# Kernel tuning notes

Hardware: AMD Instinct MI355X
Metric: run time of the kernel (lower is better)

## Reference

```python
import jax, jax.numpy as jnp
import numpy as np

N_NODES = 50000
N_EDGES = 1000000
IN_C = 64
OUT_C = 64
N_TYPES = 4


def setup_inputs() -> dict:
    key = jax.random.key(0)
    k_x, k_ei, k_et, k_w, k_rw, k_rb = jax.random.split(key, 6)
    x = jax.random.normal(k_x, (N_NODES, IN_C), dtype=jnp.float32)
    edge_index = jax.random.randint(k_ei, (2, N_EDGES), 0, N_NODES, dtype=jnp.int64)
    edge_type = jax.random.randint(k_et, (N_EDGES,), 0, N_TYPES, dtype=jnp.int64)
    # xavier_uniform for weight: bound = sqrt(6/(in+out))
    bound_w = float(np.sqrt(6.0 / (IN_C + OUT_C)))
    weight = jax.random.uniform(k_w, (N_TYPES, IN_C, OUT_C), minval=-bound_w, maxval=bound_w, dtype=jnp.float32)
    # nn.Linear default init: kaiming_uniform-ish, U(-1/sqrt(in), 1/sqrt(in))
    bound_l = float(1.0 / np.sqrt(IN_C))
    root_w = jax.random.uniform(k_rw, (IN_C, OUT_C), minval=-bound_l, maxval=bound_l, dtype=jnp.float32)
    root_b = jax.random.uniform(k_rb, (OUT_C,), minval=-bound_l, maxval=bound_l, dtype=jnp.float32)
    return {"x": x, "edge_index": edge_index, "edge_type": edge_type,
            "weight": weight, "root_w": root_w, "root_b": root_b}


def reference(x, edge_index, edge_type, weight, root_w, root_b):
    src, dst = edge_index[0], edge_index[1]
    x_src = x[src]                                   # [E, in]
    # Per-type GEMM + masked select; avoids materializing weight[edge_type] ([E,in,out]).
    msgs = jnp.zeros((x_src.shape[0], weight.shape[2]), dtype=x.dtype)
    for t in range(weight.shape[0]):                 # small fixed type count
        sel = (edge_type == t)[:, None]
        msgs = msgs + jnp.where(sel, x_src @ weight[t], 0.0)
    # Scatter-add messages to destination nodes.
    agg = jax.ops.segment_sum(msgs, dst, num_segments=x.shape[0])  # [N, out]
    return agg + x @ root_w + root_b
```

## Files before the change

### kernel.cpp

```cpp
#include <hip/hip_runtime.h>

#define NT 64
#define NBMAX1 1024
#define CAPB 2048
#define CHUNK 4096
#define FTHR 512

typedef short bf16x8 __attribute__((ext_vector_type(8)));
typedef float f32x4  __attribute__((ext_vector_type(4)));

__device__ __forceinline__ unsigned short f2bf(float f) {
    unsigned u = __builtin_bit_cast(unsigned, f);
    unsigned r = (u + 0x7fffu + ((u >> 16) & 1u)) >> 16;
    return (unsigned short)r;
}
__device__ __forceinline__ float bf2f(unsigned short h) {
    return __builtin_bit_cast(float, (unsigned)h << 16);
}
__device__ __forceinline__ unsigned pack2(float a, float b) {
    return (unsigned)f2bf(a) | ((unsigned)f2bf(b) << 16);
}

__global__ __launch_bounds__(FTHR) void ph_kernel(
    const float* __restrict__ weight, const float* __restrict__ root_w,
    unsigned short* __restrict__ wt,
    const int* __restrict__ ei, int* __restrict__ counts,
    int n_edges, int nb, int nblk)
{
    const int tid = threadIdx.x;
    int g = blockIdx.x * FTHR + tid;
    if (g < 5 * 4096) {
        int m = g >> 12, rem = g & 4095, c = rem >> 6, k = rem & 63;
        float v = (m < 4) ? weight[m * 4096 + k * 64 + c] : root_w[k * 64 + c];
        int byte = m * 8192 + c * 128 + ((k * 2) ^ ((c & 7) << 4));
        wt[byte >> 1] = f2bf(v);
    }
    if (blockIdx.x >= nblk) return;

    __shared__ int lh[NBMAX1];
    for (int i = tid; i < nb; i += FTHR) lh[i] = 0;
    __syncthreads();
    const int lo = blockIdx.x * CHUNK;
    const int hi = min(lo + CHUNK, n_edges);
    for (int e = lo + tid; e < hi; e += FTHR)
        atomicAdd(&lh[ei[n_edges + e] >> 6], 1);
    __syncthreads();
    for (int i = tid; i < nb; i += FTHR)
        counts[(size_t)blockIdx.x * nb + i] = lh[i];
}

__global__ __launch_bounds__(256) void scanw_kernel(
    const int* __restrict__ counts, int* __restrict__ starts,
    int* __restrict__ cursor, int nb, int nblk)
{
    if (blockIdx.x == 0 && threadIdx.x == 0) cursor[nb] = 0;
    const int w    = (blockIdx.x * 256 + threadIdx.x) >> 6;
    const int lane = threadIdx.x & 63;
    if (w >= nb) return;
    const int b = w;
    int base = 0;
    for (int r = 0; r * 64 < nblk; ++r) {
        int i = r * 64 + lane;
        int c = (i < nblk) ? counts[(size_t)i * nb + b] : 0;
        int s = c;
        #pragma unroll
        for (int d = 1; d < 64; d <<= 1) {
            int u = __shfl_up(s, d, 64);
            if (lane >= d) s += u;
        }
        if (i < nblk) starts[(size_t)i * nb + b] = base + s - c;
        base += __shfl(s, 63, 64);
    }
    if (lane == 0) cursor[b] = base;
}

__global__ __launch_bounds__(FTHR) void fused_fg_kernel(
    const float* __restrict__ x, const uint4* __restrict__ wt4,
    const float* __restrict__ root_b,
    float* __restrict__ out, unsigned short* __restrict__ y, int n_nodes,
    const int* __restrict__ ei, const int* __restrict__ et,
    const int* __restrict__ starts, int* __restrict__ cursor,
    int2* __restrict__ spill, unsigned* __restrict__ payload,
    int n_edges, int nb, int nblk, int ssh, int tsh)
{
    __shared__ __align__(16) char smem[57344];
    const int tid = threadIdx.x;

    if (blockIdx.x < nblk) {
        unsigned*       pl   = (unsigned*)smem;
        unsigned short* bkt  = (unsigned short*)(pl + CHUNK);
        int*            lh   = (int*)(bkt + CHUNK);
        int*            loff = lh + NBMAX1;
        int*            tsum = loff + NBMAX1 + 1;

        const int blk = blockIdx.x;
        const int lo  = blk * CHUNK;
        const int hi  = min(lo + CHUNK, n_edges);
        const int n   = hi - lo;

        for (int i = tid; i < nb; i += FTHR) lh[i] = 0;
        __syncthreads();
        for (int i = tid; i < n; i += FTHR)
            atomicAdd(&lh[ei[n_edges + lo + i] >> 6], 1);
        __syncthreads();

        const int bins  = (nb + FTHR - 1) / FTHR;
        const int base_ = tid * bins;
        int s = 0;
        for (int j = 0; j < bins; ++j) {
            int idx = base_ + j;
            if (idx < nb) s += lh[idx];
        }
        tsum[tid] = s;
        __syncthreads();
        for (int d = 1; d < FTHR; d <<= 1) {
            int v = (tid >= d) ? tsum[tid - d] : 0;
            __syncthreads();
            tsum[tid] += v;
            __syncthreads();
        }
        int run = (tid == 0) ? 0 : tsum[tid - 1];
        for (int j = 0; j < bins; ++j) {
            int idx = base_ + j;
            if (idx < nb) { loff[idx] = run; run += lh[idx]; }
        }
        __syncthreads();
        for (int i = tid; i < nb; i += FTHR) lh[i] = 0;
        __syncthreads();

        for (int i = tid; i < n; i += FTHR) {
            int e   = lo + i;
            int src = ei[e];
            int dn  = ei[n_edges + e];
            int t   = et[e];
            int b   = dn >> 6;
            int r   = atomicAdd(&lh[b], 1);
            int slot = loff[b] + r;
            pl[slot]  = (unsigned)src | ((unsigned)(dn & 63) << ssh)
                      | ((unsigned)t << tsh);
            bkt[slot] = (unsigned short)b;
        }
        __syncthreads();

        const int* __restrict__ srow = starts + (size_t)blk * nb;
        for (int i = tid; i < n; i += FTHR) {
            int b    = bkt[i];
            int rank = srow[b] + (i - loff[b]);
            unsigned v = pl[i];
            if (rank < CAPB) {
                payload[(size_t)b * CAPB + rank] = v;
            } else {
                int sp = atomicAdd(&cursor[nb], 1);
                spill[sp] = make_int2(b, (int)v);
            }
        }
        return;
    }

    uint4* lds4 = (uint4*)smem;
    const int node0 = (blockIdx.x - nblk) * 128;

    for (int i = tid; i < 2560; i += FTHR) lds4[1024 + i] = wt4[i];

    {
        int n    = tid >> 2;
        int kq   = tid & 3;
        int node = node0 + n;
        uint4 p0, p1;
        if (node < n_nodes) {
            const float4* src = reinterpret_cast<const float4*>(x)
                                + (size_t)node * 16 + kq * 4;
            float4 f0 = src[0], f1 = src[1], f2 = src[2], f3 = src[3];
            p0.x = pack2(f0.x, f0.y); p0.y = pack2(f0.z, f0.w);
            p0.z = pack2(f1.x, f1.y); p0.w = pack2(f1.z, f1.w);
            p1.x = pack2(f2.x, f2.y); p1.y = pack2(f2.z, f2.w);
            p1.z = pack2(f3.x, f3.y); p1.w = pack2(f3.z, f3.w);
        } else {
            p0 = make_uint4(0, 0, 0, 0);
            p1 = p0;
        }
        int s0 = (kq * 2) ^ (n & 7);
        lds4[n * 8 + s0]       = p0;
        lds4[n * 8 + (s0 ^ 1)] = p1;
    }
    __syncthreads();

    const int wv = tid >> 6;
    const int l  = tid & 63;
    const int lo = l & 15;
    const int hi = l >> 4;

    const int arow = (wv >> 2) * 64 + (wv & 3) * 16 + lo;
    bf16x8 xb0 = *reinterpret_cast<const bf16x8*>(
        &lds4[arow * 8 + ((0 + hi) ^ (arow & 7))]);
    bf16x8 xb1 = *reinterpret_cast<const bf16x8*>(
        &lds4[arow * 8 + ((4 + hi) ^ (arow & 7))]);

    const int node   = node0 + arow;
    const bool valid = (node < n_nodes);

    for (int m = 0; m < 5; ++m) {
        f32x4 acc[4];
        #pragma unroll
        for (int j = 0; j < 4; ++j)
            acc[j] = (f32x4){0.f, 0.f, 0.f, 0.f};

        #pragma unroll
        for (int j = 0; j < 4; ++j) {
            int c     = j * 16 + lo;
            int bbase = 1024 + m * 512 + c * 8;
            bf16x8 w0 = *reinterpret_cast<const bf16x8*>(
                &lds4[bbase + ((0 + hi) ^ (c & 7))]);
            acc[j] = __builtin_amdgcn_mfma_f32_16x16x32_bf16(w0, xb0, acc[j], 0, 0, 0);
            bf16x8 w1 = *reinterpret_cast<const bf16x8*>(
                &lds4[bbase + ((4 + hi) ^ (c & 7))]);
            acc[j] = __builtin_amdgcn_mfma_f32_16x16x32_bf16(w1, xb1, acc[j], 0, 0, 0);
        }

        if (m < 4) {
            if (valid) {
                unsigned short* __restrict__ ym = y + (size_t)m * n_nodes * 64;
                #pragma unroll
                for (int j = 0; j < 4; ++j) {
                    uint2 o;
                    o.x = pack2(acc[j][0], acc[j][1]);
                    o.y = pack2(acc[j][2], acc[j][3]);
                    *reinterpret_cast<uint2*>(
                        &ym[(size_t)node * 64 + j * 16 + hi * 4]) = o;
                }
            }
        } else {
            if (valid) {
                #pragma unroll
                for (int j = 0; j < 4; ++j) {
                    float4 rb = reinterpret_cast<const float4*>(root_b)[j * 4 + hi];
                    float4 o  = make_float4(acc[j][0] + rb.x, acc[j][1] + rb.y,
                                            acc[j][2] + rb.z, acc[j][3] + rb.w);
                    *reinterpret_cast<float4*>(
                        &out[(size_t)node * 64 + j * 16 + hi * 4]) = o;
                }
            }
        }
    }
}

__global__ __launch_bounds__(1024) void gatherb5_kernel(
    const int* __restrict__ cursor, const unsigned* __restrict__ payload,
    const int2* __restrict__ spill,
    const unsigned short* __restrict__ y, float* __restrict__ out,
    int n_nodes, int nb, int ssh, int tsh)
{
    __shared__ unsigned raw[CAPB];
    __shared__ unsigned srt[CAPB];
    __shared__ int hist[64];
    __shared__ int hoff[65];

    const int tid = threadIdx.x;
    const int b   = blockIdx.x;
    const int n_in = min(cursor[b], CAPB);
    const unsigned* __restrict__ pl_base = payload + (size_t)b * CAPB;

    if (tid < 64) hist[tid] = 0;
    __syncthreads();
    for (int i = tid; i < n_in; i += 1024) {
        unsigned pl = pl_base[i];
        raw[i] = pl;
        atomicAdd(&hist[(pl >> ssh) & 63], 1);
    }
    __syncthreads();
    if (tid < 64) {
        int v = hist[tid];
        int s = v;
        #pragma unroll
        for (int d = 1; d < 64; d <<= 1) {
            int u = __shfl_up(s, d, 64);
            if (tid >= d) s += u;
        }
        hoff[tid] = s - v;
        if (tid == 63) hoff[64] = s;
        hist[tid] = 0;
    }
    __syncthreads();
    for (int i = tid; i < n_in; i += 1024) {
        unsigned pl = raw[i];
        int lnode = (pl >> ssh) & 63;
        int r = atomicAdd(&hist[lnode], 1);
        srt[hoff[lnode] + r] = pl;
    }
    __syncthreads();

    const int g    = tid >> 4;
    const int cq   = tid & 15;
    const int node = b * 64 + g;
    const unsigned smask = (1u << ssh) - 1;
    const ushort4* __restrict__ y4 = reinterpret_cast<const ushort4*>(y);

    float4 acc = make_float4(0.f, 0.f, 0.f, 0.f);
    const int s0 = hoff[g];
    const int s1 = hoff[g + 1];
    int p = s0;
    for (; p + 1 < s1; p += 2) {
        unsigned pl0 = srt[p];
        unsigned pl1 = srt[p + 1];
        ushort4 v0 = y4[((long)(pl0 >> tsh) * n_nodes + (pl0 & smask)) * 16 + cq];
        ushort4 v1 = y4[((long)(pl1 >> tsh) * n_nodes + (pl1 & smask)) * 16 + cq];
        acc.x += bf2f(v0.x) + bf2f(v1.x);
        acc.y += bf2f(v0.y) + bf2f(v1.y);
        acc.z += bf2f(v0.z) + bf2f(v1.z);
        acc.w += bf2f(v0.w) + bf2f(v1.w);
    }
    if (p < s1) {
        unsigned pl = srt[p];
        ushort4 v = y4[((long)(pl >> tsh) * n_nodes + (pl & smask)) * 16 + cq];
        acc.x += bf2f(v.x); acc.y += bf2f(v.y);
        acc.z += bf2f(v.z); acc.w += bf2f(v.w);
    }

    const int S = cursor[nb];
    for (int i = 0; i < S; ++i) {
        int2 sp = spill[i];
        if (sp.x == b) {
            unsigned v = (unsigned)sp.y;
            if ((int)((v >> ssh) & 63) == g) {
                int src = (int)(v & smask);
                int t   = (int)(v >> tsh);
                ushort4 w = y4[((long)t * n_nodes + src) * 16 + cq];
                acc.x += bf2f(w.x); acc.y += bf2f(w.y);
                acc.z += bf2f(w.z); acc.w += bf2f(w.w);
            }
        }
    }

    if (node < n_nodes) {
        float4* o  = reinterpret_cast<float4*>(out) + (long)node * 16 + cq;
        float4 cur = *o;
        cur.x += acc.x; cur.y += acc.y; cur.z += acc.z; cur.w += acc.w;
        *o = cur;
    }
}

__global__ __launch_bounds__(256) void gemm_fused2_kernel(
    const float* __restrict__ x, const float* __restrict__ weight,
    const float* __restrict__ root_w, const float* __restrict__ root_b,
    float* __restrict__ out, unsigned short* __restrict__ y, int n_nodes)
{
    __shared__ unsigned short xsT[64][72];
    __shared__ float ws[64][72];
    const int tid   = threadIdx.x;
    const int node0 = blockIdx.x * 64;
    #pragma unroll
    for (int i = 0; i < 4; ++i) {
        int v    = tid + i * 256;
        int r    = v >> 4;
        int cq   = v & 15;
        int node = node0 + r;
        float4 x4 = (node < n_nodes)
                        ? reinterpret_cast<const float4*>(x)[(size_t)node * 16 + cq]
                        : make_float4(0.f, 0.f, 0.f, 0.f);
        xsT[cq * 4 + 0][r] = f2bf(x4.x);
        xsT[cq * 4 + 1][r] = f2bf(x4.y);
        xsT[cq * 4 + 2][r] = f2bf(x4.z);
        xsT[cq * 4 + 3][r] = f2bf(x4.w);
    }
    const int ng = tid & 31;
    const int cg = tid >> 5;
    float bias[8];
    #pragma unroll
    for (int j = 0; j < 8; ++j) bias[j] = root_b[cg * 8 + j];
    for (int m = 0; m < 5; ++m) {
        const float* __restrict__ W = (m < 4) ? (weight + m * 4096) : root_w;
        __syncthreads();
        #pragma unroll
        for (int i = 0; i < 4; ++i) {
            int v  = tid + i * 256;
            int r  = v >> 4;
            int cq = v & 15;
            float4 w4 = reinterpret_cast<const float4*>(W)[v];
            ws[r][cq * 4 + 0] = w4.x; ws[r][cq * 4 + 1] = w4.y;
            ws[r][cq * 4 + 2] = w4.z; ws[r][cq * 4 + 3] = w4.w;
        }
        __syncthreads();
        float acc[2][8];
        #pragma unroll
        for (int i = 0; i < 2; ++i)
            #pragma unroll
            for (int j = 0; j < 8; ++j) acc[i][j] = 0.f;
        #pragma unroll 4
        for (int k = 0; k < 64; ++k) {
            unsigned xu = *reinterpret_cast<const unsigned*>(&xsT[k][ng * 2]);
            float xv0 = __builtin_bit_cast(float, xu << 16);
            float xv1 = __builtin_bit_cast(float, xu & 0xffff0000u);
            float4 wa = *reinterpret_cast<const float4*>(&ws[k][cg * 8]);
            float4 wb = *reinterpret_cast<const float4*>(&ws[k][cg * 8 + 4]);
            float wv[8] = {wa.x, wa.y, wa.z, wa.w, wb.x, wb.y, wb.z, wb.w};
            #pragma unroll
            for (int j = 0; j < 8; ++j) {
                acc[0][j] += xv0 * wv[j];
                acc[1][j] += xv1 * wv[j];
            }
        }
        #pragma unroll
        for (int i = 0; i < 2; ++i) {
            int node = node0 + ng * 2 + i;
            if (node >= n_nodes) continue;
            if (m < 4) {
                uint4 o;
                o.x = pack2(acc[i][0], acc[i][1]);
                o.y = pack2(acc[i][2], acc[i][3]);
                o.z = pack2(acc[i][4], acc[i][5]);
                o.w = pack2(acc[i][6], acc[i][7]);
                *reinterpret_cast<uint4*>(
                    &y[((size_t)m * n_nodes + node) * 64 + cg * 8]) = o;
            } else {
                float4 oa = make_float4(acc[i][0] + bias[0], acc[i][1] + bias[1],
                                        acc[i][2] + bias[2], acc[i][3] + bias[3]);
                float4 ob = make_float4(acc[i][4] + bias[4], acc[i][5] + bias[5],
                                        acc[i][6] + bias[6], acc[i][7] + bias[7]);
                reinterpret_cast<float4*>(&out[(size_t)node * 64 + cg * 8])[0] = oa;
                reinterpret_cast<float4*>(&out[(size_t)node * 64 + cg * 8])[1] = ob;
            }
        }
    }
}

__global__ __launch_bounds__(256) void scatter_kernel(
    const int* __restrict__ ei, const int* __restrict__ et,
    const unsigned short* __restrict__ y, float* __restrict__ out,
    int n_edges, int n_nodes)
{
    long idx = (long)blockIdx.x * blockDim.x + threadIdx.x;
    if (idx >= (long)n_edges * 16) return;
    int e  = (int)(idx >> 4);
    int cq = (int)(idx & 15);
    int src  = ei[e];
    int dstn = ei[n_edges + e];
    int t    = et[e];
    ushort4 v = reinterpret_cast<const ushort4*>(y)[((long)t * n_nodes + src) * 16 + cq];
    float* o = out + (long)dstn * 64 + cq * 4;
    atomicAdd(o + 0, bf2f(v.x));
    atomicAdd(o + 1, bf2f(v.y));
    atomicAdd(o + 2, bf2f(v.z));
    atomicAdd(o + 3, bf2f(v.w));
}

__global__ __launch_bounds__(256) void gemm_root_kernel(
    const float* __restrict__ x, const float* __restrict__ root_w,
    const float* __restrict__ root_b, float* __restrict__ out, int n_nodes)
{
    __shared__ float xs[NT][65];
    __shared__ float ws[64][65];
    const int tid   = threadIdx.x;
    const int node0 = blockIdx.x * NT;
    #pragma unroll
    for (int i = 0; i < 4; ++i) {
        int v  = tid + i * 256;
        int r  = v >> 4;
        int cq = v & 15;
        float4 w4 = reinterpret_cast<const float4*>(root_w)[v];
        ws[r][cq * 4 + 0] = w4.x; ws[r][cq * 4 + 1] = w4.y;
        ws[r][cq * 4 + 2] = w4.z; ws[r][cq * 4 + 3] = w4.w;
        int node = node0 + r;
        float4 x4 = (node < n_nodes)
                        ? reinterpret_cast<const float4*>(x)[node * 16 + cq]
                        : make_float4(0.f, 0.f, 0.f, 0.f);
        xs[r][cq * 4 + 0] = x4.x; xs[r][cq * 4 + 1] = x4.y;
        xs[r][cq * 4 + 2] = x4.z; xs[r][cq * 4 + 3] = x4.w;
    }
    __syncthreads();
    const int tc = (tid & 15) * 4;
    const int tr = (tid >> 4) * 4;
    float acc[4][4];
    #pragma unroll
    for (int i = 0; i < 4; ++i)
        #pragma unroll
        for (int j = 0; j < 4; ++j) acc[i][j] = 0.f;
    #pragma unroll 4
    for (int k = 0; k < 64; ++k) {
        float xv[4], wv[4];
        #pragma unroll
        for (int i = 0; i < 4; ++i) xv[i] = xs[tr + i][k];
        #pragma unroll
        for (int j = 0; j < 4; ++j) wv[j] = ws[k][tc + j];
        #pragma unroll
        for (int i = 0; i < 4; ++i)
            #pragma unroll
            for (int j = 0; j < 4; ++j) acc[i][j] += xv[i] * wv[j];
    }
    #pragma unroll
    for (int i = 0; i < 4; ++i) {
        int node = node0 + tr + i;
        if (node < n_nodes) {
            float4 o = make_float4(acc[i][0] + root_b[tc + 0], acc[i][1] + root_b[tc + 1],
                                   acc[i][2] + root_b[tc + 2], acc[i][3] + root_b[tc + 3]);
            reinterpret_cast<float4*>(out)[node * 16 + (tc >> 2)] = o;
        }
    }
}

__global__ __launch_bounds__(256) void edge_direct_kernel(
    const float* __restrict__ x, const int* __restrict__ ei,
    const int* __restrict__ et, const float* __restrict__ weight,
    float* __restrict__ out, int n_edges)
{
    int gwave  = (int)((blockIdx.x * (long)blockDim.x + threadIdx.x) >> 6);
    int lane   = threadIdx.x & 63;
    int nwaves = (int)(((long)gridDim.x * blockDim.x) >> 6);
    for (int e = gwave; e < n_edges; e += nwaves) {
        int src  = ei[e];
        int dstn = ei[n_edges + e];
        int t    = et[e];
        float xv = x[src * 64 + lane];
        const float* __restrict__ W = weight + t * 4096;
        float acc = 0.f;
        #pragma unroll 8
        for (int k = 0; k < 64; ++k) {
            float xk = __shfl(xv, k);
            acc += xk * W[k * 64 + lane];
        }
        atomicAdd(&out[(long)dstn * 64 + lane], acc);
    }
}

extern "C" void kernel_launch(void* const* d_in, const int* in_sizes, int n_in,
                              void* d_out, int out_size, void* d_ws, size_t ws_size,
                              hipStream_t stream) {
    const float* x      = (const float*)d_in[0];
    const int*   ei     = (const int*)d_in[1];
    const int*   et     = (const int*)d_in[2];
    const float* weight = (const float*)d_in[3];
    const float* root_w = (const float*)d_in[4];
    const float* root_b = (const float*)d_in[5];
    float* out = (float*)d_out;

    const int n_nodes = in_sizes[0] / 64;
    const int n_edges = in_sizes[2];
    const int nb      = (n_nodes + 63) >> 6;
    const int nblk    = (n_edges + CHUNK - 1) / CHUNK;

    int ssh = 1;
    while ((1 << ssh) < n_nodes) ++ssh;
    const int tsh = ssh + 6;

    const size_t wt_bytes = 5 * 4096 * sizeof(unsigned short);
    const size_t y_bytes  = (size_t)4 * n_nodes * 64 * sizeof(unsigned short);
    const size_t b_bytes  = wt_bytes + y_bytes +
        ((size_t)nb + 1 + 2 * (size_t)nblk * nb + (size_t)nb * CAPB
         + 2 * (size_t)n_edges) * 4;

    const int gemm_blocks = (n_nodes + 127) / 128;

    if (nb <= NBMAX1 && tsh + 2 <= 32 && ws_size >= b_bytes) {
        unsigned short* wt      = (unsigned short*)d_ws;
        unsigned short* y       = (unsigned short*)((char*)d_ws + wt_bytes);
        int*            cursor  = (int*)((char*)d_ws + wt_bytes + y_bytes);
        int*            counts  = cursor + nb + 1;
        int*            starts  = counts + (size_t)nblk * nb;
        unsigned*       payload = (unsigned*)(starts + (size_t)nblk * nb);
        int2*           spill   = (int2*)(payload + (size_t)nb * CAPB);

        const int ph_blocks = max(nblk, (5 * 4096 + FTHR - 1) / FTHR);
        ph_kernel<<<ph_blocks, FTHR, 0, stream>>>(
            weight, root_w, wt, ei, counts, n_edges, nb, nblk);
        scanw_kernel<<<(nb * 64 + 255) / 256, 256, 0, stream>>>(
            counts, starts, cursor, nb, nblk);
        fused_fg_kernel<<<nblk + gemm_blocks, FTHR, 0, stream>>>(
            x, (const uint4*)wt, root_b, out, y, n_nodes,
            ei, et, starts, cursor, spill, payload,
            n_edges, nb, nblk, ssh, tsh);
        gatherb5_kernel<<<nb, 1024, 0, stream>>>(
            cursor, payload, spill, y, out, n_nodes, nb, ssh, tsh);
    } else if (ws_size >= y_bytes) {
        unsigned short* y = (unsigned short*)d_ws;
        gemm_fused2_kernel<<<(n_nodes + 63) / 64, 256, 0, stream>>>(
            x, weight, root_w, root_b, out, y, n_nodes);
        long total  = (long)n_edges * 16;
        int  blocks = (int)((total + 255) / 256);
        scatter_kernel<<<blocks, 256, 0, stream>>>(ei, et, y, out, n_edges, n_nodes);
    } else {
        gemm_root_kernel<<<(n_nodes + NT - 1) / NT, 256, 0, stream>>>(
            x, root_w, root_b, out, n_nodes);
        edge_direct_kernel<<<4096, 256, 0, stream>>>(x, ei, et, weight, out, n_edges);
    }
}
```

Before: 65.14 us.

## Fuse four-kernel pipeline into one cooperative persistent kernel with grid syncs

Replaces the four launches (histogram/weight prep, scan, bucket+GEMM, gather) with a single cooperative mega-kernel that loops over work items and uses grid.sync between phases. The aim is to remove launch gaps and tail effects between the dependent stages. In exchange the grid is capped at 512 persistent blocks, so each block handles several chunks serially. The gather phase now uses 512 threads per bucket instead of 1024, and the grid barriers add their own cost. The launch path also makes several host-side attribute and occupancy queries on every call.

```diff
diff --git a/kernel.cpp b/kernel.cpp
--- a/kernel.cpp
+++ b/kernel.cpp
@@ -1,4 +1,6 @@
 #include <hip/hip_runtime.h>
+#include <hip/hip_cooperative_groups.h>
+namespace cg = cooperative_groups;
 
 #define NT 64
 #define NBMAX1 1024
@@ -19,6 +21,327 @@
 }
 __device__ __forceinline__ unsigned pack2(float a, float b) {
     return (unsigned)f2bf(a) | ((unsigned)f2bf(b) << 16);
+}
+
+__global__ __launch_bounds__(FTHR) void mega_kernel(
+    const float* x, const float* weight, const float* root_w,
+    const float* root_b, float* out, unsigned short* wt,
+    unsigned short* y, const int* ei, const int* et,
+    int* counts, int* starts, int* cursor, int2* spill,
+    unsigned* payload, int n_nodes, int n_edges, int nb, int nblk,
+    int gemm_tiles, int ssh, int tsh)
+{
+    cg::grid_group grid = cg::this_grid();
+    __shared__ __align__(16) char smem[57344];
+    const int tid  = threadIdx.x;
+    const int nthr = gridDim.x * FTHR;
+
+    for (int g = blockIdx.x * FTHR + tid; g < 5 * 4096; g += nthr) {
+        int m = g >> 12, rem = g & 4095, c = rem >> 6, k = rem & 63;
+        float v = (m < 4) ? weight[m * 4096 + k * 64 + c] : root_w[k * 64 + c];
+        int byte = m * 8192 + c * 128 + ((k * 2) ^ ((c & 7) << 4));
+        wt[byte >> 1] = f2bf(v);
+    }
+    if (blockIdx.x == 0 && tid == 0) cursor[nb] = 0;
+    {
+        int* lh = (int*)smem;
+        for (int c = blockIdx.x; c < nblk; c += gridDim.x) {
+            __syncthreads();
+            for (int i = tid; i < nb; i += FTHR) lh[i] = 0;
+            __syncthreads();
+            const int lo = c * CHUNK;
+            const int hi = min(lo + CHUNK, n_edges);
+            for (int e = lo + tid; e < hi; e += FTHR)
+                atomicAdd(&lh[ei[n_edges + e] >> 6], 1);
+            __syncthreads();
+            for (int i = tid; i < nb; i += FTHR)
+                counts[(size_t)c * nb + i] = lh[i];
+        }
+    }
+    grid.sync();
+
+    {
+        const int lane = tid & 63;
+        for (int b = blockIdx.x * 8 + (tid >> 6); b < nb; b += gridDim.x * 8) {
+            int base = 0;
+            for (int r = 0; r * 64 < nblk; ++r) {
+                int i = r * 64 + lane;
+                int c = (i < nblk) ? counts[(size_t)i * nb + b] : 0;
+                int s = c;
+                #pragma unroll
+                for (int d = 1; d < 64; d <<= 1) {
+                    int u = __shfl_up(s, d, 64);
+                    if (lane >= d) s += u;
+                }
+                if (i < nblk) starts[(size_t)i * nb + b] = base + s - c;
+                base += __shfl(s, 63, 64);
+            }
+            if (lane == 0) cursor[b] = base;
+        }
+    }
+    grid.sync();
+
+    const int nit = nblk + gemm_tiles;
+    for (int it = blockIdx.x; it < nit; it += gridDim.x) {
+        __syncthreads();
+        if (it < nblk) {
+            unsigned*       pl   = (unsigned*)smem;
+            unsigned short* bkt  = (unsigned short*)(pl + CHUNK);
+            int*            lh   = (int*)(bkt + CHUNK);
+            int*            loff = lh + NBMAX1;
+            int*            tsum = loff + NBMAX1 + 1;
+
+            const int blk = it;
+            const int lo  = blk * CHUNK;
+            const int hi  = min(lo + CHUNK, n_edges);
+            const int n   = hi - lo;
+
+            for (int i = tid; i < nb; i += FTHR) lh[i] = 0;
+            __syncthreads();
+            for (int i = tid; i < n; i += FTHR)
+                atomicAdd(&lh[ei[n_edges + lo + i] >> 6], 1);
+            __syncthreads();
+
+            const int bins  = (nb + FTHR - 1) / FTHR;
+            const int base_ = tid * bins;
+            int s = 0;
+            for (int j = 0; j < bins; ++j) {
+                int idx = base_ + j;
+                if (idx < nb) s += lh[idx];
+            }
+            tsum[tid] = s;
+            __syncthreads();
+            for (int d = 1; d < FTHR; d <<= 1) {
+                int v = (tid >= d) ? tsum[tid - d] : 0;
+                __syncthreads();
+                tsum[tid] += v;
+                __syncthreads();
+            }
+            int run = (tid == 0) ? 0 : tsum[tid - 1];
+            for (int j = 0; j < bins; ++j) {
+                int idx = base_ + j;
+                if (idx < nb) { loff[idx] = run; run += lh[idx]; }
+            }
+            __syncthreads();
+            for (int i = tid; i < nb; i += FTHR) lh[i] = 0;
+            __syncthreads();
+
+            for (int i = tid; i < n; i += FTHR) {
+                int e   = lo + i;
+                int src = ei[e];
+                int dn  = ei[n_edges + e];
+                int t   = et[e];
+                int b   = dn >> 6;
+                int r   = atomicAdd(&lh[b], 1);
+                int slot = loff[b] + r;
+                pl[slot]  = (unsigned)src | ((unsigned)(dn & 63) << ssh)
+                          | ((unsigned)t << tsh);
+                bkt[slot] = (unsigned short)b;
+            }
+            __syncthreads();
+
+            const int* srow = starts + (size_t)blk * nb;
+            for (int i = tid; i < n; i += FTHR) {
+                int b    = bkt[i];
+                int rank = srow[b] + (i - loff[b]);
+                unsigned v = pl[i];
+                if (rank < CAPB) {
+                    payload[(size_t)b * CAPB + rank] = v;
+                } else {
+                    int sp = atomicAdd(&cursor[nb], 1);
+                    spill[sp] = make_int2(b, (int)v);
+                }
+            }
+        } else {
+            uint4* lds4 = (uint4*)smem;
+            const uint4* wt4 = (const uint4*)wt;
+            const int node0 = (it - nblk) * 128;
+
+            for (int i = tid; i < 2560; i += FTHR) lds4[1024 + i] = wt4[i];
+            {
+                int n    = tid >> 2;
+                int kq   = tid & 3;
+                int node = node0 + n;
+                uint4 p0, p1;
+                if (node < n_nodes) {
+                    const float4* src = reinterpret_cast<const float4*>(x)
+                                        + (size_t)node * 16 + kq * 4;
+                    float4 f0 = src[0], f1 = src[1], f2 = src[2], f3 = src[3];
+                    p0.x = pack2(f0.x, f0.y); p0.y = pack2(f0.z, f0.w);
+                    p0.z = pack2(f1.x, f1.y); p0.w = pack2(f1.z, f1.w);
+                    p1.x = pack2(f2.x, f2.y); p1.y = pack2(f2.z, f2.w);
+                    p1.z = pack2(f3.x, f3.y); p1.w = pack2(f3.z, f3.w);
+                } else {
+                    p0 = make_uint4(0, 0, 0, 0);
+                    p1 = p0;
+                }
+                int s0 = (kq * 2) ^ (n & 7);
+                lds4[n * 8 + s0]       = p0;
+                lds4[n * 8 + (s0 ^ 1)] = p1;
+            }
+            __syncthreads();
+
+            const int wv = tid >> 6;
+            const int l  = tid & 63;
+            const int lo = l & 15;
+            const int hi = l >> 4;
+
+            const int arow = (wv >> 2) * 64 + (wv & 3) * 16 + lo;
+            bf16x8 xb0 = *reinterpret_cast<const bf16x8*>(
+                &lds4[arow * 8 + ((0 + hi) ^ (arow & 7))]);
+            bf16x8 xb1 = *reinterpret_cast<const bf16x8*>(
+                &lds4[arow * 8 + ((4 + hi) ^ (arow & 7))]);
+
+            const int node   = node0 + arow;
+            const bool valid = (node < n_nodes);
+
+            for (int m = 0; m < 5; ++m) {
+                f32x4 acc[4];
+                #pragma unroll
+                for (int j = 0; j < 4; ++j)
+                    acc[j] = (f32x4){0.f, 0.f, 0.f, 0.f};
+                #pragma unroll
+                for (int j = 0; j < 4; ++j) {
+                    int c     = j * 16 + lo;
+                    int bbase = 1024 + m * 512 + c * 8;
+                    bf16x8 w0 = *reinterpret_cast<const bf16x8*>(
+                        &lds4[bbase + ((0 + hi) ^ (c & 7))]);
+                    acc[j] = __builtin_amdgcn_mfma_f32_16x16x32_bf16(w0, xb0, acc[j], 0, 0, 0);
+                    bf16x8 w1 = *reinterpret_cast<const bf16x8*>(
+                        &lds4[bbase + ((4 + hi) ^ (c & 7))]);
+                    acc[j] = __builtin_amdgcn_mfma_f32_16x16x32_bf16(w1, xb1, acc[j], 0, 0, 0);
+                }
+                if (m < 4) {
+                    if (valid) {
+                        unsigned short* ym = y + (size_t)m * n_nodes * 64;
+                        #pragma unroll
+                        for (int j = 0; j < 4; ++j) {
+                            uint2 o;
+                            o.x = pack2(acc[j][0], acc[j][1]);
+                            o.y = pack2(acc[j][2], acc[j][3]);
+                            *reinterpret_cast<uint2*>(
+                                &ym[(size_t)node * 64 + j * 16 + hi * 4]) = o;
+                        }
+                    }
+                } else {
+                    if (valid) {
+                        #pragma unroll
+                        for (int j = 0; j < 4; ++j) {
+                            float4 rb = reinterpret_cast<const float4*>(root_b)[j * 4 + hi];
+                            float4 o  = make_float4(acc[j][0] + rb.x, acc[j][1] + rb.y,
+                                                    acc[j][2] + rb.z, acc[j][3] + rb.w);
+                            *reinterpret_cast<float4*>(
+                                &out[(size_t)node * 64 + j * 16 + hi * 4]) = o;
+                        }
+                    }
+                }
+            }
+        }
+    }
+    grid.sync();
+
+    for (int b = blockIdx.x; b < nb; b += gridDim.x) {
+        __syncthreads();
+        unsigned* raw  = (unsigned*)smem;
+        unsigned* srt  = raw + CAPB;
+        int*      hist = (int*)(srt + CAPB);
+        int*      hoff = hist + 64;
+
+        const int n_in = min(cursor[b], CAPB);
+        const unsigned* pl_base = payload + (size_t)b * CAPB;
+
+        if (tid < 64) hist[tid] = 0;
+        __syncthreads();
+        for (int i = tid; i < n_in; i += FTHR) {
+            unsigned pl = pl_base[i];
+            raw[i] = pl;
+            atomicAdd(&hist[(pl >> ssh) & 63], 1);
+        }
+        __syncthreads();
+        if (tid < 64) {
+            int v = hist[tid];
+            int s = v;
+            #pragma unroll
+            for (int d = 1; d < 64; d <<= 1) {
+                int u = __shfl_up(s, d, 64);
+                if (tid >= d) s += u;
+            }
+            hoff[tid] = s - v;
+            if (tid == 63) hoff[64] = s;
+            hist[tid] = 0;
+        }
+        __syncthreads();
+        for (int i = tid; i < n_in; i += FTHR) {
+            unsigned pl = raw[i];
+            int lnode = (pl >> ssh) & 63;
+            int r = atomicAdd(&hist[lnode], 1);
+            srt[hoff[lnode] + r] = pl;
+        }
+        __syncthreads();
+
+        const int g    = tid >> 3;
+        const int co   = (tid & 7) * 8;
+        const int node = b * 64 + g;
+        const unsigned smask = (1u << ssh) - 1;
+        const uint4* y4 = reinterpret_cast<const uint4*>(y);
+
+        float acc[8];
+        #pragma unroll
+        for (int j = 0; j < 8; ++j) acc[j] = 0.f;
+
+        const int s0 = hoff[g];
+        const int s1 = hoff[g + 1];
+        int p = s0;
+        for (; p + 1 < s1; p += 2) {
+            unsigned pl0 = srt[p];
+            unsigned pl1 = srt[p + 1];
+            uint4 v0 = y4[(((size_t)(pl0 >> tsh) * n_nodes + (pl0 & smask)) * 64 + co) >> 3];
+            uint4 v1 = y4[(((size_t)(pl1 >> tsh) * n_nodes + (pl1 & smask)) * 64 + co) >> 3];
+            acc[0] += __builtin_bit_cast(float, v0.x << 16) + __builtin_bit_cast(float, v1.x << 16);
+            acc[1] += __builtin_bit_cast(float, v0.x & 0xffff0000u) + __builtin_bit_cast(float, v1.x & 0xffff0000u);
+            acc[2] += __builtin_bit_cast(float, v0.y << 16) + __builtin_bit_cast(float, v1.y << 16);
+            acc[3] += __builtin_bit_cast(float, v0.y & 0xffff0000u) + __builtin_bit_cast(float, v1.y & 0xffff0000u);
+            acc[4] += __builtin_bit_cast(float, v0.z << 16) + __builtin_bit_cast(float, v1.z << 16);
+            acc[5] += __builtin_bit_cast(float, v0.z & 0xffff0000u) + __builtin_bit_cast(float, v1.z & 0xffff0000u);
+            acc[6] += __builtin_bit_cast(float, v0.w << 16) + __builtin_bit_cast(float, v1.w << 16);
+            acc[7] += __builtin_bit_cast(float, v0.w & 0xffff0000u) + __builtin_bit_cast(float, v1.w & 0xffff0000u);
+        }
+        if (p < s1) {
+            unsigned pl = srt[p];
+            uint4 v = y4[(((size_t)(pl >> tsh) * n_nodes + (pl & smask)) * 64 + co) >> 3];
+            acc[0] += __builtin_bit_cast(float, v.x << 16);
+            acc[1] += __builtin_bit_cast(float, v.x & 0xffff0000u);
+            acc[2] += __builtin_bit_cast(float, v.y << 16);
+            acc[3] += __builtin_bit_cast(float, v.y & 0xffff0000u);
+            acc[4] += __builtin_bit_cast(float, v.z << 16);
+            acc[5] += __builtin_bit_cast(float, v.z & 0xffff0000u);
+            acc[6] += __builtin_bit_cast(float, v.w << 16);
+            acc[7] += __builtin_bit_cast(float, v.w & 0xffff0000u);
+        }
+
+        const int S = cursor[nb];
+        for (int i = 0; i < S; ++i) {
+            int2 sp = spill[i];
+            if (sp.x == b) {
+                unsigned v = (unsigned)sp.y;
+                if ((int)((v >> ssh) & 63) == g) {
+                    int src = (int)(v & smask);
+                    int t   = (int)(v >> tsh);
+                    const unsigned short* yr = y + ((size_t)t * n_nodes + src) * 64 + co;
+                    #pragma unroll
+                    for (int j = 0; j < 8; ++j) acc[j] += bf2f(yr[j]);
+                }
+            }
+        }
+
+        if (node < n_nodes) {
+            float4* o = reinterpret_cast<float4*>(out + (size_t)node * 64 + co);
+            float4 a = o[0], c2 = o[1];
+            a.x += acc[0]; a.y += acc[1]; a.z += acc[2]; a.w += acc[3];
+            c2.x += acc[4]; c2.y += acc[5]; c2.z += acc[6]; c2.w += acc[7];
+            o[0] = a; o[1] = c2;
+        }
+    }
 }
 
 __global__ __launch_bounds__(FTHR) void ph_kernel(
@@ -36,7 +359,6 @@
         wt[byte >> 1] = f2bf(v);
     }
     if (blockIdx.x >= nblk) return;
-
     __shared__ int lh[NBMAX1];
     for (int i = tid; i < nb; i += FTHR) lh[i] = 0;
     __syncthreads();
@@ -85,25 +407,21 @@
 {
     __shared__ __align__(16) char smem[57344];
     const int tid = threadIdx.x;
-
     if (blockIdx.x < nblk) {
         unsigned*       pl   = (unsigned*)smem;
         unsigned short* bkt  = (unsigned short*)(pl + CHUNK);
         int*            lh   = (int*)(bkt + CHUNK);
         int*            loff = lh + NBMAX1;
         int*            tsum = loff + NBMAX1 + 1;
-
         const int blk = blockIdx.x;
         const int lo  = blk * CHUNK;
         const int hi  = min(lo + CHUNK, n_edges);
         const int n   = hi - lo;
-
         for (int i = tid; i < nb; i += FTHR) lh[i] = 0;
         __syncthreads();
         for (int i = tid; i < n; i += FTHR)
             atomicAdd(&lh[ei[n_edges + lo + i] >> 6], 1);
         __syncthreads();
-
         const int bins  = (nb + FTHR - 1) / FTHR;
         const int base_ = tid * bins;
         int s = 0;
@@ -127,7 +445,6 @@
         __syncthreads();
         for (int i = tid; i < nb; i += FTHR) lh[i] = 0;
         __syncthreads();
-
         for (int i = tid; i < n; i += FTHR) {
             int e   = lo + i;
             int src = ei[e];
@@ -141,27 +458,19 @@
             bkt[slot] = (unsigned short)b;
         }
         __syncthreads();
-
         const int* __restrict__ srow = starts + (size_t)blk * nb;
         for (int i = tid; i < n; i += FTHR) {
             int b    = bkt[i];
             int rank = srow[b] + (i - loff[b]);
             unsigned v = pl[i];
-            if (rank < CAPB) {
-                payload[(size_t)b * CAPB + rank] = v;
-            } else {
-                int sp = atomicAdd(&cursor[nb], 1);
-                spill[sp] = make_int2(b, (int)v);
-            }
+            if (rank < CAPB) payload[(size_t)b * CAPB + rank] = v;
+            else { int sp = atomicAdd(&cursor[nb], 1); spill[sp] = make_int2(b, (int)v); }
         }
         return;
     }
-
     uint4* lds4 = (uint4*)smem;
     const int node0 = (blockIdx.x - nblk) * 128;
-
     for (int i = tid; i < 2560; i += FTHR) lds4[1024 + i] = wt4[i];
-
     {
         int n    = tid >> 2;
         int kq   = tid & 3;
@@ -175,36 +484,27 @@
             p0.z = pack2(f1.x, f1.y); p0.w = pack2(f1.z, f1.w);
             p1.x = pack2(f2.x, f2.y); p1.y = pack2(f2.z, f2.w);
             p1.z = pack2(f3.x, f3.y); p1.w = pack2(f3.z, f3.w);
-        } else {
-            p0 = make_uint4(0, 0, 0, 0);
-            p1 = p0;
-        }
+        } else { p0 = make_uint4(0, 0, 0, 0); p1 = p0; }
         int s0 = (kq * 2) ^ (n & 7);
         lds4[n * 8 + s0]       = p0;
         lds4[n * 8 + (s0 ^ 1)] = p1;
     }
     __syncthreads();
-
     const int wv = tid >> 6;
     const int l  = tid & 63;
     const int lo = l & 15;
     const int hi = l >> 4;
-
     const int arow = (wv >> 2) * 64 + (wv & 3) * 16 + lo;
     bf16x8 xb0 = *reinterpret_cast<const bf16x8*>(
         &lds4[arow * 8 + ((0 + hi) ^ (arow & 7))]);
     bf16x8 xb1 = *reinterpret_cast<const bf16x8*>(
         &lds4[arow * 8 + ((4 + hi) ^ (arow & 7))]);
-
     const int node   = node0 + arow;
     const bool valid = (node < n_nodes);
-
     for (int m = 0; m < 5; ++m) {
         f32x4 acc[4];
         #pragma unroll
-        for (int j = 0; j < 4; ++j)
-            acc[j] = (f32x4){0.f, 0.f, 0.f, 0.f};
-
+        for (int j = 0; j < 4; ++j) acc[j] = (f32x4){0.f, 0.f, 0.f, 0.f};
         #pragma unroll
         for (int j = 0; j < 4; ++j) {
             int c     = j * 16 + lo;
@@ -216,7 +516,6 @@
                 &lds4[bbase + ((4 + hi) ^ (c & 7))]);
             acc[j] = __builtin_amdgcn_mfma_f32_16x16x32_bf16(w1, xb1, acc[j], 0, 0, 0);
         }
-
         if (m < 4) {
             if (valid) {
                 unsigned short* __restrict__ ym = y + (size_t)m * n_nodes * 64;
@@ -229,16 +528,14 @@
                         &ym[(size_t)node * 64 + j * 16 + hi * 4]) = o;
                 }
             }
-        } else {
-            if (valid) {
-                #pragma unroll
-                for (int j = 0; j < 4; ++j) {
-                    float4 rb = reinterpret_cast<const float4*>(root_b)[j * 4 + hi];
-                    float4 o  = make_float4(acc[j][0] + rb.x, acc[j][1] + rb.y,
-                                            acc[j][2] + rb.z, acc[j][3] + rb.w);
-                    *reinterpret_cast<float4*>(
-                        &out[(size_t)node * 64 + j * 16 + hi * 4]) = o;
-                }
+        } else if (valid) {
+            #pragma unroll
+            for (int j = 0; j < 4; ++j) {
+                float4 rb = reinterpret_cast<const float4*>(root_b)[j * 4 + hi];
+                float4 o  = make_float4(acc[j][0] + rb.x, acc[j][1] + rb.y,
+                                        acc[j][2] + rb.z, acc[j][3] + rb.w);
+                *reinterpret_cast<float4*>(
+                    &out[(size_t)node * 64 + j * 16 + hi * 4]) = o;
             }
         }
     }
@@ -254,12 +551,10 @@
     __shared__ unsigned srt[CAPB];
     __shared__ int hist[64];
     __shared__ int hoff[65];
-
     const int tid = threadIdx.x;
     const int b   = blockIdx.x;
     const int n_in = min(cursor[b], CAPB);
     const unsigned* __restrict__ pl_base = payload + (size_t)b * CAPB;
-
     if (tid < 64) hist[tid] = 0;
     __syncthreads();
     for (int i = tid; i < n_in; i += 1024) {
@@ -288,13 +583,11 @@
         srt[hoff[lnode] + r] = pl;
     }
     __syncthreads();
-
     const int g    = tid >> 4;
     const int cq   = tid & 15;
     const int node = b * 64 + g;
     const unsigned smask = (1u << ssh) - 1;
     const ushort4* __restrict__ y4 = reinterpret_cast<const ushort4*>(y);
-
     float4 acc = make_float4(0.f, 0.f, 0.f, 0.f);
     const int s0 = hoff[g];
     const int s1 = hoff[g + 1];
@@ -315,7 +608,6 @@
         acc.x += bf2f(v.x); acc.y += bf2f(v.y);
         acc.z += bf2f(v.z); acc.w += bf2f(v.w);
     }
-
     const int S = cursor[nb];
     for (int i = 0; i < S; ++i) {
         int2 sp = spill[i];
@@ -330,117 +622,12 @@
             }
         }
     }
-
     if (node < n_nodes) {
         float4* o  = reinterpret_cast<float4*>(out) + (long)node * 16 + cq;
         float4 cur = *o;
         cur.x += acc.x; cur.y += acc.y; cur.z += acc.z; cur.w += acc.w;
         *o = cur;
     }
-}
-
-__global__ __launch_bounds__(256) void gemm_fused2_kernel(
-    const float* __restrict__ x, const float* __restrict__ weight,
-    const float* __restrict__ root_w, const float* __restrict__ root_b,
-    float* __restrict__ out, unsigned short* __restrict__ y, int n_nodes)
-{
-    __shared__ unsigned short xsT[64][72];
-    __shared__ float ws[64][72];
-    const int tid   = threadIdx.x;
-    const int node0 = blockIdx.x * 64;
-    #pragma unroll
-    for (int i = 0; i < 4; ++i) {
-        int v    = tid + i * 256;
-        int r    = v >> 4;
-        int cq   = v & 15;
-        int node = node0 + r;
-        float4 x4 = (node < n_nodes)
-                        ? reinterpret_cast<const float4*>(x)[(size_t)node * 16 + cq]
-                        : make_float4(0.f, 0.f, 0.f, 0.f);
-        xsT[cq * 4 + 0][r] = f2bf(x4.x);
-        xsT[cq * 4 + 1][r] = f2bf(x4.y);
-        xsT[cq * 4 + 2][r] = f2bf(x4.z);
-        xsT[cq * 4 + 3][r] = f2bf(x4.w);
-    }
-    const int ng = tid & 31;
-    const int cg = tid >> 5;
-    float bias[8];
-    #pragma unroll
-    for (int j = 0; j < 8; ++j) bias[j] = root_b[cg * 8 + j];
-    for (int m = 0; m < 5; ++m) {
-        const float* __restrict__ W = (m < 4) ? (weight + m * 4096) : root_w;
-        __syncthreads();
-        #pragma unroll
-        for (int i = 0; i < 4; ++i) {
-            int v  = tid + i * 256;
-            int r  = v >> 4;
-            int cq = v & 15;
-            float4 w4 = reinterpret_cast<const float4*>(W)[v];
-            ws[r][cq * 4 + 0] = w4.x; ws[r][cq * 4 + 1] = w4.y;
-            ws[r][cq * 4 + 2] = w4.z; ws[r][cq * 4 + 3] = w4.w;
-        }
-        __syncthreads();
-        float acc[2][8];
-        #pragma unroll
-        for (int i = 0; i < 2; ++i)
-            #pragma unroll
-            for (int j = 0; j < 8; ++j) acc[i][j] = 0.f;
-        #pragma unroll 4
-        for (int k = 0; k < 64; ++k) {
-            unsigned xu = *reinterpret_cast<const unsigned*>(&xsT[k][ng * 2]);
-            float xv0 = __builtin_bit_cast(float, xu << 16);
-            float xv1 = __builtin_bit_cast(float, xu & 0xffff0000u);
-            float4 wa = *reinterpret_cast<const float4*>(&ws[k][cg * 8]);
-            float4 wb = *reinterpret_cast<const float4*>(&ws[k][cg * 8 + 4]);
-            float wv[8] = {wa.x, wa.y, wa.z, wa.w, wb.x, wb.y, wb.z, wb.w};
-            #pragma unroll
-            for (int j = 0; j < 8; ++j) {
-                acc[0][j] += xv0 * wv[j];
-                acc[1][j] += xv1 * wv[j];
-            }
-        }
-        #pragma unroll
-        for (int i = 0; i < 2; ++i) {
-            int node = node0 + ng * 2 + i;
-            if (node >= n_nodes) continue;
-            if (m < 4) {
-                uint4 o;
-                o.x = pack2(acc[i][0], acc[i][1]);
-                o.y = pack2(acc[i][2], acc[i][3]);
-                o.z = pack2(acc[i][4], acc[i][5]);
-                o.w = pack2(acc[i][6], acc[i][7]);
-                *reinterpret_cast<uint4*>(
-                    &y[((size_t)m * n_nodes + node) * 64 + cg * 8]) = o;
-            } else {
-                float4 oa = make_float4(acc[i][0] + bias[0], acc[i][1] + bias[1],
-                                        acc[i][2] + bias[2], acc[i][3] + bias[3]);
-                float4 ob = make_float4(acc[i][4] + bias[4], acc[i][5] + bias[5],
-                                        acc[i][6] + bias[6], acc[i][7] + bias[7]);
-                reinterpret_cast<float4*>(&out[(size_t)node * 64 + cg * 8])[0] = oa;
-                reinterpret_cast<float4*>(&out[(size_t)node * 64 + cg * 8])[1] = ob;
-            }
-        }
-    }
-}
-
-__global__ __launch_bounds__(256) void scatter_kernel(
-    const int* __restrict__ ei, const int* __restrict__ et,
-    const unsigned short* __restrict__ y, float* __restrict__ out,
-    int n_edges, int n_nodes)
-{
-    long idx = (long)blockIdx.x * blockDim.x + threadIdx.x;
-    if (idx >= (long)n_edges * 16) return;
-    int e  = (int)(idx >> 4);
-    int cq = (int)(idx & 15);
-    int src  = ei[e];
-    int dstn = ei[n_edges + e];
-    int t    = et[e];
-    ushort4 v = reinterpret_cast<const ushort4*>(y)[((long)t * n_nodes + src) * 16 + cq];
-    float* o = out + (long)dstn * 64 + cq * 4;
-    atomicAdd(o + 0, bf2f(v.x));
-    atomicAdd(o + 1, bf2f(v.y));
-    atomicAdd(o + 2, bf2f(v.z));
-    atomicAdd(o + 3, bf2f(v.w));
 }
 
 __global__ __launch_bounds__(256) void gemm_root_kernel(
@@ -536,6 +723,7 @@
     const int n_edges = in_sizes[2];
     const int nb      = (n_nodes + 63) >> 6;
     const int nblk    = (n_edges + CHUNK - 1) / CHUNK;
+    const int gemm_tiles = (n_nodes + 127) / 128;
 
     int ssh = 1;
     while ((1 << ssh) < n_nodes) ++ssh;
@@ -546,8 +734,6 @@
     const size_t b_bytes  = wt_bytes + y_bytes +
         ((size_t)nb + 1 + 2 * (size_t)nblk * nb + (size_t)nb * CAPB
          + 2 * (size_t)n_edges) * 4;
-
-    const int gemm_blocks = (n_nodes + 127) / 128;
 
     if (nb <= NBMAX1 && tsh + 2 <= 32 && ws_size >= b_bytes) {
         unsigned short* wt      = (unsigned short*)d_ws;
@@ -558,24 +744,36 @@
         unsigned*       payload = (unsigned*)(starts + (size_t)nblk * nb);
         int2*           spill   = (int2*)(payload + (size_t)nb * CAPB);
 
-        const int ph_blocks = max(nblk, (5 * 4096 + FTHR - 1) / FTHR);
-        ph_kernel<<<ph_blocks, FTHR, 0, stream>>>(
-            weight, root_w, wt, ei, counts, n_edges, nb, nblk);
-        scanw_kernel<<<(nb * 64 + 255) / 256, 256, 0, stream>>>(
-            counts, starts, cursor, nb, nblk);
-        fused_fg_kernel<<<nblk + gemm_blocks, FTHR, 0, stream>>>(
-            x, (const uint4*)wt, root_b, out, y, n_nodes,
-            ei, et, starts, cursor, spill, payload,
-            n_edges, nb, nblk, ssh, tsh);
-        gatherb5_kernel<<<nb, 1024, 0, stream>>>(
-            cursor, payload, spill, y, out, n_nodes, nb, ssh, tsh);
-    } else if (ws_size >= y_bytes) {
-        unsigned short* y = (unsigned short*)d_ws;
-        gemm_fused2_kernel<<<(n_nodes + 63) / 64, 256, 0, stream>>>(
-            x, weight, root_w, root_b, out, y, n_nodes);
-        long total  = (long)n_edges * 16;
-        int  blocks = (int)((total + 255) / 256);
-        scatter_kernel<<<blocks, 256, 0, stream>>>(ei, et, y, out, n_edges, n_nodes);
+        int coop = 0, maxb = 0, ncu = 0, dev = 0;
+        hipGetDevice(&dev);
+        hipDeviceGetAttribute(&coop, hipDeviceAttributeCooperativeLaunch, dev);
+        hipDeviceGetAttribute(&ncu, hipDeviceAttributeMultiprocessorCount, dev);
+        hipOccupancyMaxActiveBlocksPerMultiprocessor(&maxb, mega_kernel, FTHR, 0);
+
+        if (coop && maxb > 0 && ncu > 0) {
+            int grid = maxb * ncu;
+            if (grid > 512) grid = 512;
+            void* args[] = {
+                (void*)&x, (void*)&weight, (void*)&root_w, (void*)&root_b,
+                (void*)&out, (void*)&wt, (void*)&y, (void*)&ei, (void*)&et,
+                (void*)&counts, (void*)&starts, (void*)&cursor, (void*)&spill,
+                (void*)&payload, (void*)&n_nodes, (void*)&n_edges, (void*)&nb,
+                (void*)&nblk, (void*)&gemm_tiles, (void*)&ssh, (void*)&tsh };
+            hipLaunchCooperativeKernel((const void*)mega_kernel, dim3(grid),
+                                       dim3(FTHR), args, 0, stream);
+        } else {
+            const int ph_blocks = max(nblk, (5 * 4096 + FTHR - 1) / FTHR);
+            ph_kernel<<<ph_blocks, FTHR, 0, stream>>>(
+                weight, root_w, wt, ei, counts, n_edges, nb, nblk);
+            scanw_kernel<<<(nb * 64 + 255) / 256, 256, 0, stream>>>(
+                counts, starts, cursor, nb, nblk);
+            fused_fg_kernel<<<nblk + gemm_tiles, FTHR, 0, stream>>>(
+                x, (const uint4*)wt, root_b, out, y, n_nodes,
+                ei, et, starts, cursor, spill, payload,
+                n_edges, nb, nblk, ssh, tsh);
+            gatherb5_kernel<<<nb, 1024, 0, stream>>>(
+                cursor, payload, spill, y, out, n_nodes, nb, ssh, tsh);
+        }
     } else {
         gemm_root_kernel<<<(n_nodes + NT - 1) / NT, 256, 0, stream>>>(
             x, root_w, root_b, out, n_nodes);
```

New measurement: 180.2 us. 2.77x slower.
